# Kernel optimization log

Measured on AMD Instinct MI355X. Metric: run time of the kernel, lower is better.

The kernel has to match this reference:

```python
import jax, jax.numpy as jnp
import numpy as np

N_NODES = 50000
N_EDGES = 800000
N_PRED = 100000  # pos and neg each
D_IN = 256
D_HID = 128  # hard-coded hidden width of conv1
D_OUT = 128  # out_channels


def _lin_params(key, fan_in, fan_out, dtype=jnp.float32):
    kw, kb = jax.random.split(key)
    s = 1.0 / np.sqrt(fan_in)
    W = jax.random.uniform(kw, (fan_in, fan_out), dtype, -s, s)
    b = jax.random.uniform(kb, (fan_out,), dtype, -s, s)
    return W, b


def setup_inputs() -> dict:
    key = jax.random.key(0)
    ks = jax.random.split(key, 16)
    inp = {
        "x": jax.random.normal(ks[0], (N_NODES, D_IN), jnp.float32),
        "edge_index": jax.random.randint(ks[1], (2, N_EDGES), 0, N_NODES, jnp.int64),
        "pos_edge_index": jax.random.randint(ks[2], (2, N_PRED), 0, N_NODES, jnp.int64),
        "neg_edge_index": jax.random.randint(ks[3], (2, N_PRED), 0, N_NODES, jnp.int64),
    }
    # conv1: TransformerConv(D_IN -> D_HID), heads=1, root_weight=True
    inp["Wq1"], inp["bq1"] = _lin_params(ks[4], D_IN, D_HID)
    inp["Wk1"], inp["bk1"] = _lin_params(ks[5], D_IN, D_HID)
    inp["Wv1"], inp["bv1"] = _lin_params(ks[6], D_IN, D_HID)
    inp["Ws1"], inp["bs1"] = _lin_params(ks[7], D_IN, D_HID)
    # conv2: TransformerConv(D_HID -> D_OUT)
    inp["Wq2"], inp["bq2"] = _lin_params(ks[8], D_HID, D_OUT)
    inp["Wk2"], inp["bk2"] = _lin_params(ks[9], D_HID, D_OUT)
    inp["Wv2"], inp["bv2"] = _lin_params(ks[10], D_HID, D_OUT)
    inp["Ws2"], inp["bs2"] = _lin_params(ks[11], D_HID, D_OUT)
    # final edge scorer Linear(D_OUT, 1)
    inp["Wl"], inp["bl"] = _lin_params(ks[12], D_OUT, 1)
    return inp


def _transformer_conv(x, Wq, bq, Wk, bk, Wv, bv, Ws, bs, src, dst, n_nodes):
    # PyG TransformerConv, heads=1, concat=True, root_weight=True, no edge attrs.
    C = Wq.shape[1]
    q = x @ Wq + bq  # [N, C] queries (destination side)
    k = x @ Wk + bk  # [N, C] keys (source side)
    v = x @ Wv + bv  # [N, C] values (source side)
    # per-edge attention logits, softmax normalized over incoming edges of dst
    alpha = jnp.einsum("ec,ec->e", q[dst], k[src]) / jnp.sqrt(jnp.asarray(C, x.dtype))
    amax = jax.lax.stop_gradient(jax.ops.segment_max(alpha, dst, num_segments=n_nodes))
    ex = jnp.exp(alpha - amax[dst])
    den = jax.ops.segment_sum(ex, dst, num_segments=n_nodes)
    w = ex / den[dst]  # [E]
    agg = jax.ops.segment_sum(v[src] * w[:, None], dst, num_segments=n_nodes)  # [N, C]
    return agg + (x @ Ws + bs)  # skip connection (lin_skip)


def reference(x, edge_index, pos_edge_index, neg_edge_index,
              Wq1, bq1, Wk1, bk1, Wv1, bv1, Ws1, bs1,
              Wq2, bq2, Wk2, bk2, Wv2, bv2, Ws2, bs2,
              Wl, bl):
    src, dst = edge_index[0], edge_index[1]
    h = _transformer_conv(x, Wq1, bq1, Wk1, bk1, Wv1, bv1, Ws1, bs1, src, dst, N_NODES)
    h = jax.nn.relu(h)
    h = _transformer_conv(h, Wq2, bq2, Wk2, bk2, Wv2, bv2, Ws2, bs2, src, dst, N_NODES)
    ei = jnp.concatenate([pos_edge_index, neg_edge_index], axis=-1)  # [2, 2*N_PRED]
    prod = h[ei[0]] * h[ei[1]]  # [2*N_PRED, D_OUT]
    return (prod @ Wl + bl).squeeze(-1)  # [2*N_PRED]
```

## Files before the change

### kernel.cpp

```cpp
#include <hip/hip_runtime.h>
#include <cstdint>
#include <cstddef>

#define NN 50000
#define NE 800000
#define NP 100000
#define NB 196

typedef _Float16 h8v __attribute__((ext_vector_type(8)));
typedef _Float16 h4v __attribute__((ext_vector_type(4)));
typedef float    f4v __attribute__((ext_vector_type(4)));

#define ATTN_SCALE 0.088388347648318447f

__device__ inline void load_lds16(const void* gptr, void* ldsptr) {
  __builtin_amdgcn_global_load_lds(
      (const __attribute__((address_space(1))) void*)gptr,
      (__attribute__((address_space(3))) void*)ldsptr, 16, 0, 0);
}

__global__ __launch_bounds__(256) void hist_kernel(const int* __restrict__ dst,
                                                   int* __restrict__ deg,
                                                   int* __restrict__ rank, int E) {
  int e = blockIdx.x * 256 + threadIdx.x;
  if (e < E) rank[e] = atomicAdd(&deg[dst[e]], 1);
}

__global__ __launch_bounds__(256) void scan1_kernel(const int* __restrict__ deg,
                                                    int* __restrict__ loc,
                                                    int* __restrict__ bsum, int n) {
  __shared__ int sh[256];
  int tid = threadIdx.x;
  int i = blockIdx.x * 256 + tid;
  int val = (i < n) ? deg[i] : 0;
  sh[tid] = val;
  __syncthreads();
  for (int off = 1; off < 256; off <<= 1) {
    int add = (tid >= off) ? sh[tid - off] : 0;
    __syncthreads();
    sh[tid] += add;
    __syncthreads();
  }
  if (i < n) loc[i] = sh[tid] - val;
  if (tid == 255) bsum[blockIdx.x] = sh[255];
}

__global__ __launch_bounds__(256) void scan2_kernel(int* __restrict__ bsum, int nb) {
  __shared__ int sh[256];
  int tid = threadIdx.x;
  int v = (tid < nb) ? bsum[tid] : 0;
  sh[tid] = v;
  __syncthreads();
  for (int off = 1; off < 256; off <<= 1) {
    int add = (tid >= off) ? sh[tid - off] : 0;
    __syncthreads();
    sh[tid] += add;
    __syncthreads();
  }
  if (tid < nb) bsum[tid] = sh[tid] - v;
}

__global__ __launch_bounds__(256) void scan3_kernel(const int* __restrict__ loc,
                                                    const int* __restrict__ bsum,
                                                    int* __restrict__ offs, int n, int E) {
  int i = blockIdx.x * 256 + threadIdx.x;
  if (i < n) offs[i] = loc[i] + bsum[blockIdx.x];
  if (i == 0) offs[n] = E;
}

__global__ __launch_bounds__(256) void scatter_kernel(const int* __restrict__ src,
                                                      const int* __restrict__ dst,
                                                      const int* __restrict__ offs,
                                                      const int* __restrict__ rank,
                                                      int* __restrict__ csr_src, int E) {
  int e = blockIdx.x * 256 + threadIdx.x;
  if (e < E) {
    int d = dst[e];
    csr_src[offs[d] + rank[e]] = src[e];
  }
}

__global__ __launch_bounds__(256) void cvt_f16_kernel(const float* __restrict__ X,
                                                      _Float16* __restrict__ Xf, int n4) {
  int i = blockIdx.x * 256 + threadIdx.x;
  if (i >= n4) return;
  float4 x = ((const float4*)X)[i];
  h4v o = {(_Float16)x.x, (_Float16)x.y, (_Float16)x.z, (_Float16)x.w};
  ((h4v*)Xf)[i] = o;
}

__global__ void packw_kernel(const float* __restrict__ W0, const float* __restrict__ W1,
                             const float* __restrict__ W2, const float* __restrict__ W3,
                             _Float16* __restrict__ WT, int K) {
  int n = blockIdx.x;
  int k = threadIdx.x;
  const float* W;
  switch (n >> 7) {
    case 0:  W = W0; break;
    case 1:  W = W1; break;
    case 2:  W = W2; break;
    default: W = W3; break;
  }
  int c = n & 127;
  WT[(size_t)n * K + k] = (_Float16)W[(size_t)k * 128 + c];
}

__global__ __launch_bounds__(256) void gemm_f16_kernel(
    const _Float16* __restrict__ A, int M, int K,
    const _Float16* __restrict__ BT,
    const float* __restrict__ b0, const float* __restrict__ b1,
    const float* __restrict__ b2, const float* __restrict__ b3,
    _Float16* __restrict__ O0, _Float16* __restrict__ O1,
    _Float16* __restrict__ O2, _Float16* __restrict__ O3) {
  const float* bias;
  _Float16* Oh;
  switch (blockIdx.y) {
    case 0:  bias = b0; Oh = O0; break;
    case 1:  bias = b1; Oh = O1; break;
    case 2:  bias = b2; Oh = O2; break;
    default: bias = b3; Oh = O3; break;
  }

  __shared__ _Float16 smem[16384];
  _Float16* As = smem;
  _Float16* Bs = smem + 8192;

  const int tx = threadIdx.x;
  const int w = tx >> 6;
  const int lane = tx & 63;
  const int lr = lane & 15;
  const int q = lane >> 4;
  const int wm = w >> 1, wn = w & 1;
  const int row0 = blockIdx.x * 128;
  const int col0 = blockIdx.y * 128;

  const bool isA = (w < 2);
  const int wh = w & 1;

  f4v acc[4][4];
#pragma unroll
  for (int i = 0; i < 4; ++i)
#pragma unroll
    for (int j = 0; j < 4; ++j) acc[i][j] = (f4v){0.f, 0.f, 0.f, 0.f};

  for (int k0 = 0; k0 < K; k0 += 64) {
    __syncthreads();
#pragma unroll
    for (int o = 0; o < 8; ++o) {
      int r = wh * 64 + o * 8 + (lane >> 3);
      int cl = (lane & 7) ^ (r & 7);
      const _Float16* g;
      _Float16* base;
      if (isA) {
        int gr = row0 + r;
        if (gr > M - 1) gr = M - 1;
        g = A + (size_t)gr * K + k0 + cl * 8;
        base = &As[(wh * 64 + o * 8) * 64];
      } else {
        g = BT + (size_t)(col0 + r) * K + k0 + cl * 8;
        base = &Bs[(wh * 64 + o * 8) * 64];
      }
      load_lds16(g, base);
    }
    __syncthreads();

#pragma unroll
    for (int kk = 0; kk < 2; ++kk) {
      h8v af[4], bf[4];
#pragma unroll
      for (int t = 0; t < 4; ++t) {
        int row = wm * 64 + t * 16 + lr;
        af[t] = *(const h8v*)&As[row * 64 + ((kk * 4 + q) ^ (row & 7)) * 8];
        int col = wn * 64 + t * 16 + lr;
        bf[t] = *(const h8v*)&Bs[col * 64 + ((kk * 4 + q) ^ (col & 7)) * 8];
      }
#pragma unroll
      for (int mt = 0; mt < 4; ++mt)
#pragma unroll
        for (int nt = 0; nt < 4; ++nt)
          acc[mt][nt] = __builtin_amdgcn_mfma_f32_16x16x32_f16(af[mt], bf[nt],
                                                               acc[mt][nt], 0, 0, 0);
    }
  }

#pragma unroll
  for (int half = 0; half < 2; ++half) {
    __syncthreads();
    if (wm == half) {
#pragma unroll
      for (int nt = 0; nt < 4; ++nt) {
        int col = wn * 64 + nt * 16 + lr;
        float bv = bias[col];
#pragma unroll
        for (int mt = 0; mt < 4; ++mt)
#pragma unroll
          for (int reg = 0; reg < 4; ++reg) {
            int r = mt * 16 + q * 4 + reg;
            smem[r * 128 + col] = (_Float16)(acc[mt][nt][reg] + bv);
          }
      }
    }
    __syncthreads();
#pragma unroll
    for (int i = 0; i < 4; ++i) {
      int sl = i * 256 + tx;
      int rr = sl >> 4;
      int cc = (sl & 15) * 8;
      int grow = row0 + half * 64 + rr;
      if (grow < M)
        *(h8v*)(Oh + (size_t)grow * 128 + cc) = *(const h8v*)&smem[rr * 128 + cc];
    }
  }
}

__global__ __launch_bounds__(256) void attn_fused_kernel(
    const _Float16* __restrict__ qf, const _Float16* __restrict__ kf,
    const _Float16* __restrict__ vf, const _Float16* __restrict__ sf,
    const int* __restrict__ offs, const int* __restrict__ csr_src,
    _Float16* __restrict__ hf, int n_nodes, int do_relu) {
  int node = (int)((blockIdx.x * 256u + threadIdx.x) >> 6);
  if (node >= n_nodes) return;
  int lane = threadIdx.x & 63;
  int g = lane >> 4;
  int t = lane & 15;

  h8v qv = *(const h8v*)(qf + (size_t)node * 128 + t * 8);
  int beg = offs[node], end = offs[node + 1];

  float den = 0.f;
  float acc[8];
#pragma unroll
  for (int j = 0; j < 8; ++j) acc[j] = 0.f;

  int e = beg + g;
  for (; e + 4 < end; e += 8) {
    int sn0 = csr_src[e];
    int sn1 = csr_src[e + 4];
    h8v k0 = *(const h8v*)(kf + (size_t)sn0 * 128 + t * 8);
    h8v v0 = *(const h8v*)(vf + (size_t)sn0 * 128 + t * 8);
    h8v k1 = *(const h8v*)(kf + (size_t)sn1 * 128 + t * 8);
    h8v v1 = *(const h8v*)(vf + (size_t)sn1 * 128 + t * 8);
    float p0 = 0.f, p1 = 0.f;
#pragma unroll
    for (int j = 0; j < 8; ++j) {
      p0 = fmaf((float)qv[j], (float)k0[j], p0);
      p1 = fmaf((float)qv[j], (float)k1[j], p1);
    }
    p0 += __shfl_xor(p0, 1); p1 += __shfl_xor(p1, 1);
    p0 += __shfl_xor(p0, 2); p1 += __shfl_xor(p1, 2);
    p0 += __shfl_xor(p0, 4); p1 += __shfl_xor(p1, 4);
    p0 += __shfl_xor(p0, 8); p1 += __shfl_xor(p1, 8);
    float w0 = __expf(p0 * ATTN_SCALE);
    float w1 = __expf(p1 * ATTN_SCALE);
    den += w0 + w1;
#pragma unroll
    for (int j = 0; j < 8; ++j) {
      acc[j] = fmaf(w0, (float)v0[j], acc[j]);
      acc[j] = fmaf(w1, (float)v1[j], acc[j]);
    }
  }
  if (e < end) {
    int sn0 = csr_src[e];
    h8v k0 = *(const h8v*)(kf + (size_t)sn0 * 128 + t * 8);
    h8v v0 = *(const h8v*)(vf + (size_t)sn0 * 128 + t * 8);
    float p0 = 0.f;
#pragma unroll
    for (int j = 0; j < 8; ++j) p0 = fmaf((float)qv[j], (float)k0[j], p0);
    p0 += __shfl_xor(p0, 1);
    p0 += __shfl_xor(p0, 2);
    p0 += __shfl_xor(p0, 4);
    p0 += __shfl_xor(p0, 8);
    float w0 = __expf(p0 * ATTN_SCALE);
    den += w0;
#pragma unroll
    for (int j = 0; j < 8; ++j) acc[j] = fmaf(w0, (float)v0[j], acc[j]);
  }

#pragma unroll
  for (int j = 0; j < 8; ++j) {
    acc[j] += __shfl_xor(acc[j], 16);
    acc[j] += __shfl_xor(acc[j], 32);
  }
  den += __shfl_xor(den, 16);
  den += __shfl_xor(den, 32);

  if (g == 0) {
    float inv = (end > beg) ? 1.f / den : 0.f;
    h8v sk = *(const h8v*)(sf + (size_t)node * 128 + t * 8);
    h8v of;
#pragma unroll
    for (int j = 0; j < 8; ++j) {
      float o = fmaf(acc[j], inv, (float)sk[j]);
      if (do_relu) o = fmaxf(o, 0.f);
      of[j] = (_Float16)o;
    }
    *(h8v*)(hf + (size_t)node * 128 + t * 8) = of;
  }
}

__global__ __launch_bounds__(256) void scorer_kernel(
    const _Float16* __restrict__ hf,
    const int* __restrict__ pos0, const int* __restrict__ pos1,
    const int* __restrict__ neg0, const int* __restrict__ neg1,
    const float* __restrict__ Wl, const float* __restrict__ bl,
    float* __restrict__ out, int npred) {
  int eid = (int)((blockIdx.x * 256u + threadIdx.x) >> 4);
  if (eid >= 2 * npred) return;
  int t = threadIdx.x & 15;

  int a, b;
  if (eid < npred) { a = pos0[eid]; b = pos1[eid]; }
  else             { a = neg0[eid - npred]; b = neg1[eid - npred]; }

  h8v ha = *(const h8v*)(hf + (size_t)a * 128 + t * 8);
  h8v hb = *(const h8v*)(hf + (size_t)b * 128 + t * 8);
  const float4* wp = (const float4*)(Wl + t * 8);
  float4 w0 = wp[0], w1 = wp[1];
  float wl[8] = {w0.x, w0.y, w0.z, w0.w, w1.x, w1.y, w1.z, w1.w};
  float p = 0.f;
#pragma unroll
  for (int j = 0; j < 8; ++j)
    p = fmaf((float)ha[j] * (float)hb[j], wl[j], p);
  p += __shfl_xor(p, 1);
  p += __shfl_xor(p, 2);
  p += __shfl_xor(p, 4);
  p += __shfl_xor(p, 8);
  if (t == 0) out[eid] = p + bl[0];
}

extern "C" void kernel_launch(void* const* d_in, const int* in_sizes, int n_in,
                              void* d_out, int out_size, void* d_ws, size_t ws_size,
                              hipStream_t stream) {
  const float* x   = (const float*)d_in[0];
  const int*   ei  = (const int*)d_in[1];
  const int*   pos = (const int*)d_in[2];
  const int*   neg = (const int*)d_in[3];
  const float* Wq1 = (const float*)d_in[4];  const float* bq1 = (const float*)d_in[5];
  const float* Wk1 = (const float*)d_in[6];  const float* bk1 = (const float*)d_in[7];
  const float* Wv1 = (const float*)d_in[8];  const float* bv1 = (const float*)d_in[9];
  const float* Ws1 = (const float*)d_in[10]; const float* bs1 = (const float*)d_in[11];
  const float* Wq2 = (const float*)d_in[12]; const float* bq2 = (const float*)d_in[13];
  const float* Wk2 = (const float*)d_in[14]; const float* bk2 = (const float*)d_in[15];
  const float* Wv2 = (const float*)d_in[16]; const float* bv2 = (const float*)d_in[17];
  const float* Ws2 = (const float*)d_in[18]; const float* bs2 = (const float*)d_in[19];
  const float* Wl  = (const float*)d_in[20]; const float* bl  = (const float*)d_in[21];
  float* out = (float*)d_out;

  const size_t NODE_C = (size_t)NN * 128;
  char* p = (char*)d_ws;
  _Float16* qf = (_Float16*)p; p += NODE_C * 2;
  _Float16* kf = (_Float16*)p; p += NODE_C * 2;
  _Float16* vf = (_Float16*)p; p += NODE_C * 2;
  _Float16* sf = (_Float16*)p; p += NODE_C * 2;
  _Float16* h1 = (_Float16*)p; p += NODE_C * 2;
  _Float16* h2 = (_Float16*)p; p += NODE_C * 2;
  _Float16* Xf = (_Float16*)p; p += (size_t)NN * 256 * 2;
  _Float16* WT1 = (_Float16*)p; p += 512 * 256 * 2;
  _Float16* WT2 = (_Float16*)p; p += 512 * 128 * 2;
  int* rank    = (int*)p;      p += (size_t)NE * 4;
  int* deg     = (int*)p;      p += (size_t)NN * 4;
  int* loc     = (int*)p;      p += (size_t)NN * 4;
  int* bsum    = (int*)p;      p += 256 * 4;
  int* offs    = (int*)p;      p += (size_t)(NN + 8) * 4;
  int* csr_src = (int*)p;      p += (size_t)NE * 4;

  const int* e_src = ei;
  const int* e_dst = ei + NE;

  hipMemsetAsync(deg, 0, NN * sizeof(int), stream);
  hist_kernel<<<(NE + 255) / 256, 256, 0, stream>>>(e_dst, deg, rank, NE);
  scan1_kernel<<<NB, 256, 0, stream>>>(deg, loc, bsum, NN);
  scan2_kernel<<<1, 256, 0, stream>>>(bsum, NB);
  scan3_kernel<<<NB, 256, 0, stream>>>(loc, bsum, offs, NN, NE);
  scatter_kernel<<<(NE + 255) / 256, 256, 0, stream>>>(e_src, e_dst, offs, rank,
                                                       csr_src, NE);

  cvt_f16_kernel<<<(NN * 256 / 4 + 255) / 256, 256, 0, stream>>>(x, Xf, NN * 256 / 4);
  packw_kernel<<<512, 256, 0, stream>>>(Wq1, Wk1, Wv1, Ws1, WT1, 256);
  packw_kernel<<<512, 128, 0, stream>>>(Wq2, Wk2, Wv2, Ws2, WT2, 128);

  dim3 ggrid((NN + 127) / 128, 4);
  int attn_blocks = (NN * 64 + 255) / 256;

  gemm_f16_kernel<<<ggrid, 256, 0, stream>>>(Xf, NN, 256, WT1,
                                             bq1, bk1, bv1, bs1, qf, kf, vf, sf);
  attn_fused_kernel<<<attn_blocks, 256, 0, stream>>>(
      qf, kf, vf, sf, offs, csr_src, h1, NN, 1);

  gemm_f16_kernel<<<ggrid, 256, 0, stream>>>(h1, NN, 128, WT2,
                                             bq2, bk2, bv2, bs2, qf, kf, vf, sf);
  attn_fused_kernel<<<attn_blocks, 256, 0, stream>>>(
      qf, kf, vf, sf, offs, csr_src, h2, NN, 0);

  scorer_kernel<<<(2 * NP * 16 + 255) / 256, 256, 0, stream>>>(
      h2, pos, pos + NP, neg, neg + NP, Wl, bl, out, NP);
}
```

Baseline: 386.1 us.

## Interleave K/V rows, widen GEMM to all four projections per block, unroll attention

Keys and values are stored interleaved per node in one buffer, so each edge gather reads one contiguous 512-byte row instead of two separate rows. The projection GEMM now computes all four Q/K/V/skip outputs in one 512-thread block, loading each A tile once instead of four times. That needs larger shared memory and more accumulator registers, which may lower occupancy. The attention loop processes four edges per group per iteration for more memory-level parallelism, and the two weight-packing launches are merged into one.

```diff
diff --git a/kernel.cpp b/kernel.cpp
--- a/kernel.cpp
+++ b/kernel.cpp
@@ -89,133 +89,149 @@
   ((h4v*)Xf)[i] = o;
 }
 
-__global__ void packw_kernel(const float* __restrict__ W0, const float* __restrict__ W1,
-                             const float* __restrict__ W2, const float* __restrict__ W3,
-                             _Float16* __restrict__ WT, int K) {
-  int n = blockIdx.x;
+__global__ __launch_bounds__(256) void packw_kernel(
+    const float* __restrict__ Wq1, const float* __restrict__ Wk1,
+    const float* __restrict__ Wv1, const float* __restrict__ Ws1,
+    const float* __restrict__ Wq2, const float* __restrict__ Wk2,
+    const float* __restrict__ Wv2, const float* __restrict__ Ws2,
+    _Float16* __restrict__ WT1, _Float16* __restrict__ WT2) {
+  int b = blockIdx.x;
   int k = threadIdx.x;
-  const float* W;
-  switch (n >> 7) {
-    case 0:  W = W0; break;
-    case 1:  W = W1; break;
-    case 2:  W = W2; break;
-    default: W = W3; break;
-  }
-  int c = n & 127;
-  WT[(size_t)n * K + k] = (_Float16)W[(size_t)k * 128 + c];
-}
-
-__global__ __launch_bounds__(256) void gemm_f16_kernel(
+  if (b < 512) {
+    int n = b;
+    const float* W;
+    switch (n >> 7) {
+      case 0:  W = Wq1; break;
+      case 1:  W = Wk1; break;
+      case 2:  W = Wv1; break;
+      default: W = Ws1; break;
+    }
+    WT1[(size_t)n * 256 + k] = (_Float16)W[(size_t)k * 128 + (n & 127)];
+  } else if (k < 128) {
+    int n = b - 512;
+    const float* W;
+    switch (n >> 7) {
+      case 0:  W = Wq2; break;
+      case 1:  W = Wk2; break;
+      case 2:  W = Wv2; break;
+      default: W = Ws2; break;
+    }
+    WT2[(size_t)n * 128 + k] = (_Float16)W[(size_t)k * 128 + (n & 127)];
+  }
+}
+
+__global__ __launch_bounds__(512) void gemm_all_kernel(
     const _Float16* __restrict__ A, int M, int K,
     const _Float16* __restrict__ BT,
-    const float* __restrict__ b0, const float* __restrict__ b1,
-    const float* __restrict__ b2, const float* __restrict__ b3,
-    _Float16* __restrict__ O0, _Float16* __restrict__ O1,
-    _Float16* __restrict__ O2, _Float16* __restrict__ O3) {
-  const float* bias;
-  _Float16* Oh;
-  switch (blockIdx.y) {
-    case 0:  bias = b0; Oh = O0; break;
-    case 1:  bias = b1; Oh = O1; break;
-    case 2:  bias = b2; Oh = O2; break;
-    default: bias = b3; Oh = O3; break;
-  }
-
-  __shared__ _Float16 smem[16384];
-  _Float16* As = smem;
-  _Float16* Bs = smem + 8192;
+    const float* __restrict__ bq, const float* __restrict__ bk,
+    const float* __restrict__ bv, const float* __restrict__ bs,
+    _Float16* __restrict__ Oq, _Float16* __restrict__ Okv,
+    _Float16* __restrict__ Os) {
+  __shared__ _Float16 As[128 * 64];
+  __shared__ _Float16 Bs[512 * 64];
 
   const int tx = threadIdx.x;
   const int w = tx >> 6;
   const int lane = tx & 63;
   const int lr = lane & 15;
   const int q = lane >> 4;
-  const int wm = w >> 1, wn = w & 1;
+  const int wm = w >> 2;
+  const int wn = w & 3;
   const int row0 = blockIdx.x * 128;
-  const int col0 = blockIdx.y * 128;
-
-  const bool isA = (w < 2);
-  const int wh = w & 1;
-
-  f4v acc[4][4];
+
+  f4v acc[4][8];
 #pragma unroll
   for (int i = 0; i < 4; ++i)
 #pragma unroll
-    for (int j = 0; j < 4; ++j) acc[i][j] = (f4v){0.f, 0.f, 0.f, 0.f};
+    for (int j = 0; j < 8; ++j) acc[i][j] = (f4v){0.f, 0.f, 0.f, 0.f};
 
   for (int k0 = 0; k0 < K; k0 += 64) {
     __syncthreads();
 #pragma unroll
+    for (int o = 0; o < 2; ++o) {
+      int i = o * 8 + w;
+      int r = i * 8 + (lane >> 3);
+      int cl = (lane & 7) ^ (r & 7);
+      int gr = row0 + r;
+      if (gr > M - 1) gr = M - 1;
+      load_lds16(A + (size_t)gr * K + k0 + cl * 8, &As[i * 8 * 64]);
+    }
+#pragma unroll
     for (int o = 0; o < 8; ++o) {
-      int r = wh * 64 + o * 8 + (lane >> 3);
+      int i = o * 8 + w;
+      int r = i * 8 + (lane >> 3);
       int cl = (lane & 7) ^ (r & 7);
-      const _Float16* g;
-      _Float16* base;
-      if (isA) {
-        int gr = row0 + r;
-        if (gr > M - 1) gr = M - 1;
-        g = A + (size_t)gr * K + k0 + cl * 8;
-        base = &As[(wh * 64 + o * 8) * 64];
-      } else {
-        g = BT + (size_t)(col0 + r) * K + k0 + cl * 8;
-        base = &Bs[(wh * 64 + o * 8) * 64];
-      }
-      load_lds16(g, base);
+      load_lds16(BT + (size_t)r * K + k0 + cl * 8, &Bs[i * 8 * 64]);
     }
     __syncthreads();
 
 #pragma unroll
     for (int kk = 0; kk < 2; ++kk) {
-      h8v af[4], bf[4];
+      h8v af[4], bf[8];
 #pragma unroll
       for (int t = 0; t < 4; ++t) {
         int row = wm * 64 + t * 16 + lr;
-        af[t] = *(const h8v*)&As[row * 64 + ((kk * 4 + q) ^ (row & 7)) * 8];
-        int col = wn * 64 + t * 16 + lr;
-        bf[t] = *(const h8v*)&Bs[col * 64 + ((kk * 4 + q) ^ (col & 7)) * 8];
+        af[t] = *(const h8v*)&As[row * 64 + (((kk * 4 + q) ^ (row & 7)) * 8)];
       }
 #pragma unroll
+      for (int u = 0; u < 8; ++u) {
+        int col = wn * 128 + u * 16 + lr;
+        bf[u] = *(const h8v*)&Bs[col * 64 + (((kk * 4 + q) ^ (col & 7)) * 8)];
+      }
+#pragma unroll
       for (int mt = 0; mt < 4; ++mt)
 #pragma unroll
-        for (int nt = 0; nt < 4; ++nt)
+        for (int nt = 0; nt < 8; ++nt)
           acc[mt][nt] = __builtin_amdgcn_mfma_f32_16x16x32_f16(af[mt], bf[nt],
                                                                acc[mt][nt], 0, 0, 0);
     }
   }
 
+  const float* bp = (wn == 0) ? bq : (wn == 1) ? bk : (wn == 2) ? bv : bs;
 #pragma unroll
   for (int half = 0; half < 2; ++half) {
     __syncthreads();
     if (wm == half) {
 #pragma unroll
-      for (int nt = 0; nt < 4; ++nt) {
-        int col = wn * 64 + nt * 16 + lr;
-        float bv = bias[col];
+      for (int nt = 0; nt < 8; ++nt) {
+        int col = wn * 128 + nt * 16 + lr;
+        float bval = bp[nt * 16 + lr];
 #pragma unroll
         for (int mt = 0; mt < 4; ++mt)
 #pragma unroll
           for (int reg = 0; reg < 4; ++reg) {
             int r = mt * 16 + q * 4 + reg;
-            smem[r * 128 + col] = (_Float16)(acc[mt][nt][reg] + bv);
+            Bs[r * 512 + col] = (_Float16)(acc[mt][nt][reg] + bval);
           }
       }
     }
     __syncthreads();
 #pragma unroll
-    for (int i = 0; i < 4; ++i) {
-      int sl = i * 256 + tx;
-      int rr = sl >> 4;
-      int cc = (sl & 15) * 8;
+    for (int i = 0; i < 8; ++i) {
+      int sl = i * 512 + tx;
+      int rr = sl >> 6;
+      int c8 = sl & 63;
+      int col = c8 * 8;
       int grow = row0 + half * 64 + rr;
-      if (grow < M)
-        *(h8v*)(Oh + (size_t)grow * 128 + cc) = *(const h8v*)&smem[rr * 128 + cc];
+      if (grow < M) {
+        int p = c8 >> 4;
+        int cp = col & 127;
+        _Float16* dst;
+        switch (p) {
+          case 0:  dst = Oq  + (size_t)grow * 128 + cp;       break;
+          case 1:  dst = Okv + (size_t)grow * 256 + cp;       break;
+          case 2:  dst = Okv + (size_t)grow * 256 + 128 + cp; break;
+          default: dst = Os  + (size_t)grow * 128 + cp;       break;
+        }
+        *(h8v*)dst = *(const h8v*)&Bs[rr * 512 + col];
+      }
     }
   }
 }
 
 __global__ __launch_bounds__(256) void attn_fused_kernel(
-    const _Float16* __restrict__ qf, const _Float16* __restrict__ kf,
-    const _Float16* __restrict__ vf, const _Float16* __restrict__ sf,
+    const _Float16* __restrict__ qf, const _Float16* __restrict__ kvf,
+    const _Float16* __restrict__ sf,
     const int* __restrict__ offs, const int* __restrict__ csr_src,
     _Float16* __restrict__ hf, int n_nodes, int do_relu) {
   int node = (int)((blockIdx.x * 256u + threadIdx.x) >> 6);
@@ -233,43 +249,56 @@
   for (int j = 0; j < 8; ++j) acc[j] = 0.f;
 
   int e = beg + g;
-  for (; e + 4 < end; e += 8) {
+  for (; e + 12 < end; e += 16) {
     int sn0 = csr_src[e];
     int sn1 = csr_src[e + 4];
-    h8v k0 = *(const h8v*)(kf + (size_t)sn0 * 128 + t * 8);
-    h8v v0 = *(const h8v*)(vf + (size_t)sn0 * 128 + t * 8);
-    h8v k1 = *(const h8v*)(kf + (size_t)sn1 * 128 + t * 8);
-    h8v v1 = *(const h8v*)(vf + (size_t)sn1 * 128 + t * 8);
-    float p0 = 0.f, p1 = 0.f;
+    int sn2 = csr_src[e + 8];
+    int sn3 = csr_src[e + 12];
+    const _Float16* r0 = kvf + (size_t)sn0 * 256 + t * 8;
+    const _Float16* r1 = kvf + (size_t)sn1 * 256 + t * 8;
+    const _Float16* r2 = kvf + (size_t)sn2 * 256 + t * 8;
+    const _Float16* r3 = kvf + (size_t)sn3 * 256 + t * 8;
+    h8v k0 = *(const h8v*)r0, v0 = *(const h8v*)(r0 + 128);
+    h8v k1 = *(const h8v*)r1, v1 = *(const h8v*)(r1 + 128);
+    h8v k2 = *(const h8v*)r2, v2 = *(const h8v*)(r2 + 128);
+    h8v k3 = *(const h8v*)r3, v3 = *(const h8v*)(r3 + 128);
+    float p0 = 0.f, p1 = 0.f, p2 = 0.f, p3 = 0.f;
 #pragma unroll
     for (int j = 0; j < 8; ++j) {
       p0 = fmaf((float)qv[j], (float)k0[j], p0);
       p1 = fmaf((float)qv[j], (float)k1[j], p1);
-    }
-    p0 += __shfl_xor(p0, 1); p1 += __shfl_xor(p1, 1);
-    p0 += __shfl_xor(p0, 2); p1 += __shfl_xor(p1, 2);
-    p0 += __shfl_xor(p0, 4); p1 += __shfl_xor(p1, 4);
-    p0 += __shfl_xor(p0, 8); p1 += __shfl_xor(p1, 8);
+      p2 = fmaf((float)qv[j], (float)k2[j], p2);
+      p3 = fmaf((float)qv[j], (float)k3[j], p3);
+    }
+#pragma unroll
+    for (int o = 1; o < 16; o <<= 1) {
+      p0 += __shfl_xor(p0, o);
+      p1 += __shfl_xor(p1, o);
+      p2 += __shfl_xor(p2, o);
+      p3 += __shfl_xor(p3, o);
+    }
     float w0 = __expf(p0 * ATTN_SCALE);
     float w1 = __expf(p1 * ATTN_SCALE);
-    den += w0 + w1;
+    float w2 = __expf(p2 * ATTN_SCALE);
+    float w3 = __expf(p3 * ATTN_SCALE);
+    den += (w0 + w1) + (w2 + w3);
 #pragma unroll
     for (int j = 0; j < 8; ++j) {
       acc[j] = fmaf(w0, (float)v0[j], acc[j]);
       acc[j] = fmaf(w1, (float)v1[j], acc[j]);
-    }
-  }
-  if (e < end) {
+      acc[j] = fmaf(w2, (float)v2[j], acc[j]);
+      acc[j] = fmaf(w3, (float)v3[j], acc[j]);
+    }
+  }
+  for (; e < end; e += 4) {
     int sn0 = csr_src[e];
-    h8v k0 = *(const h8v*)(kf + (size_t)sn0 * 128 + t * 8);
-    h8v v0 = *(const h8v*)(vf + (size_t)sn0 * 128 + t * 8);
+    const _Float16* r0 = kvf + (size_t)sn0 * 256 + t * 8;
+    h8v k0 = *(const h8v*)r0, v0 = *(const h8v*)(r0 + 128);
     float p0 = 0.f;
 #pragma unroll
     for (int j = 0; j < 8; ++j) p0 = fmaf((float)qv[j], (float)k0[j], p0);
-    p0 += __shfl_xor(p0, 1);
-    p0 += __shfl_xor(p0, 2);
-    p0 += __shfl_xor(p0, 4);
-    p0 += __shfl_xor(p0, 8);
+#pragma unroll
+    for (int o = 1; o < 16; o <<= 1) p0 += __shfl_xor(p0, o);
     float w0 = __expf(p0 * ATTN_SCALE);
     den += w0;
 #pragma unroll
@@ -348,13 +377,12 @@
 
   const size_t NODE_C = (size_t)NN * 128;
   char* p = (char*)d_ws;
-  _Float16* qf = (_Float16*)p; p += NODE_C * 2;
-  _Float16* kf = (_Float16*)p; p += NODE_C * 2;
-  _Float16* vf = (_Float16*)p; p += NODE_C * 2;
-  _Float16* sf = (_Float16*)p; p += NODE_C * 2;
-  _Float16* h1 = (_Float16*)p; p += NODE_C * 2;
-  _Float16* h2 = (_Float16*)p; p += NODE_C * 2;
-  _Float16* Xf = (_Float16*)p; p += (size_t)NN * 256 * 2;
+  _Float16* qf  = (_Float16*)p; p += NODE_C * 2;
+  _Float16* kvf = (_Float16*)p; p += NODE_C * 4;
+  _Float16* sf  = (_Float16*)p; p += NODE_C * 2;
+  _Float16* h1  = (_Float16*)p; p += NODE_C * 2;
+  _Float16* h2  = (_Float16*)p; p += NODE_C * 2;
+  _Float16* Xf  = (_Float16*)p; p += (size_t)NN * 256 * 2;
   _Float16* WT1 = (_Float16*)p; p += 512 * 256 * 2;
   _Float16* WT2 = (_Float16*)p; p += 512 * 128 * 2;
   int* rank    = (int*)p;      p += (size_t)NE * 4;
@@ -376,21 +404,21 @@
                                                        csr_src, NE);
 
   cvt_f16_kernel<<<(NN * 256 / 4 + 255) / 256, 256, 0, stream>>>(x, Xf, NN * 256 / 4);
-  packw_kernel<<<512, 256, 0, stream>>>(Wq1, Wk1, Wv1, Ws1, WT1, 256);
-  packw_kernel<<<512, 128, 0, stream>>>(Wq2, Wk2, Wv2, Ws2, WT2, 128);
-
-  dim3 ggrid((NN + 127) / 128, 4);
+  packw_kernel<<<1024, 256, 0, stream>>>(Wq1, Wk1, Wv1, Ws1, Wq2, Wk2, Wv2, Ws2,
+                                         WT1, WT2);
+
+  int ggrid = (NN + 127) / 128;
   int attn_blocks = (NN * 64 + 255) / 256;
 
-  gemm_f16_kernel<<<ggrid, 256, 0, stream>>>(Xf, NN, 256, WT1,
-                                             bq1, bk1, bv1, bs1, qf, kf, vf, sf);
+  gemm_all_kernel<<<ggrid, 512, 0, stream>>>(Xf, NN, 256, WT1,
+                                             bq1, bk1, bv1, bs1, qf, kvf, sf);
   attn_fused_kernel<<<attn_blocks, 256, 0, stream>>>(
-      qf, kf, vf, sf, offs, csr_src, h1, NN, 1);
-
-  gemm_f16_kernel<<<ggrid, 256, 0, stream>>>(h1, NN, 128, WT2,
-                                             bq2, bk2, bv2, bs2, qf, kf, vf, sf);
+      qf, kvf, sf, offs, csr_src, h1, NN, 1);
+
+  gemm_all_kernel<<<ggrid, 512, 0, stream>>>(h1, NN, 128, WT2,
+                                             bq2, bk2, bv2, bs2, qf, kvf, sf);
   attn_fused_kernel<<<attn_blocks, 256, 0, stream>>>(
-      qf, kf, vf, sf, offs, csr_src, h2, NN, 0);
+      qf, kvf, sf, offs, csr_src, h2, NN, 0);
 
   scorer_kernel<<<(2 * NP * 16 + 255) / 256, 256, 0, stream>>>(
       h2, pos, pos + NP, neg, neg + NP, Wl, bl, out, NP);
```

Measured after the change: 383.8 us. No clear change (-0.6%).
